# Kernel tuning notes

Measured on AMD Instinct MI355X. Metric: run time of the kernel, lower is better.

## Reference

```python
import jax, jax.numpy as jnp
import numpy as np

B, LQ, LKV, H, D, HS = 8, 32, 4096, 16, 64, 1024
ROPE_THETA = 10000.0
MAX_POS = 2080


def setup_inputs() -> dict:
    key = jax.random.key(0)
    ks = jax.random.split(key, 7)
    scale = 0.02
    return {
        "hidden_states": jax.random.normal(ks[0], (B, LQ, HS), dtype=jnp.float32),
        "encoder_hidden_states": jax.random.normal(ks[1], (B, LKV, HS), dtype=jnp.float32),
        "position_ids_q": jax.random.randint(ks[2], (B, LQ), 0, MAX_POS, dtype=jnp.int64),
        "Wq": jax.random.normal(ks[3], (HS, HS), dtype=jnp.float32) * scale,
        "Wk": jax.random.normal(ks[4], (HS, HS), dtype=jnp.float32) * scale,
        "Wv": jax.random.normal(ks[5], (HS, HS), dtype=jnp.float32) * scale,
        "Wo": jax.random.normal(ks[6], (HS, HS), dtype=jnp.float32) * scale,
    }


def _rotate_half(x):
    x1, x2 = jnp.split(x, 2, axis=-1)
    return jnp.concatenate([-x2, x1], axis=-1)


def _rope_cos_sin(position_ids):
    # LLaMA-style rotary embedding: inv_freq over even dims, emb = [freqs, freqs]
    inv_freq = 1.0 / (ROPE_THETA ** (jnp.arange(0, D, 2, dtype=jnp.float32) / D))
    freqs = position_ids.astype(jnp.float32)[..., None] * inv_freq  # [B, LQ, D/2]
    emb = jnp.concatenate([freqs, freqs], axis=-1)                  # [B, LQ, D]
    # broadcast over heads: [B, 1, LQ, D]
    return jnp.cos(emb)[:, None], jnp.sin(emb)[:, None]


def reference(hidden_states, encoder_hidden_states, position_ids_q, Wq, Wk, Wv, Wo):
    bsz, q_len, _ = hidden_states.shape
    kv_len = encoder_hidden_states.shape[1]
    # projections (weights stored [in, out])
    q = hidden_states @ Wq                       # [B, LQ, HS]
    k = encoder_hidden_states @ Wk               # [B, LKV, HS]
    v = encoder_hidden_states @ Wv               # [B, LKV, HS]
    # split heads -> [B, H, L, D]
    q = q.reshape(bsz, q_len, H, D).transpose(0, 2, 1, 3)
    k = k.reshape(bsz, kv_len, H, D).transpose(0, 2, 1, 3)
    v = v.reshape(bsz, kv_len, H, D).transpose(0, 2, 1, 3)
    # RoPE applied to QUERY ONLY (per original module)
    cos, sin = _rope_cos_sin(position_ids_q)
    q = q * cos + _rotate_half(q) * sin
    # scaled dot-product cross attention
    scores = jnp.einsum("bhqd,bhkd->bhqk", q, k) / jnp.sqrt(jnp.asarray(D, q.dtype))
    attn = jax.nn.softmax(scores, axis=-1)
    out = jnp.einsum("bhqk,bhkd->bhqd", attn, v)  # [B, H, LQ, D]
    out = out.transpose(0, 2, 1, 3).reshape(bsz, q_len, HS)
    return out @ Wo
```

## Files before the change

kernel.cpp:

```cpp
#include <hip/hip_runtime.h>


typedef float  f32x4  __attribute__((ext_vector_type(4)));
typedef __bf16 bf16x8 __attribute__((ext_vector_type(8)));

__device__ __forceinline__ ushort f2b(float x) {
  union { float f; unsigned u; } v; v.f = x;
  unsigned r = (v.u + 0x7fffu + ((v.u >> 16) & 1u)) >> 16;
  return (ushort)r;
}
__device__ __forceinline__ float b2f(ushort h) {
  union { unsigned u; float f; } v; v.u = ((unsigned)h) << 16; return v.f;
}
__device__ __forceinline__ void unpack2(unsigned v, float& lo, float& hi) {
  union { unsigned u; float f; } a, b;
  a.u = v << 16; b.u = v & 0xffff0000u;
  lo = a.f; hi = b.f;
}
__device__ __forceinline__ unsigned packb(float a, float b) {
  return (unsigned)f2b(a) | ((unsigned)f2b(b) << 16);
}
__device__ __forceinline__ int swz(int r) { return (r & 3) ^ ((r >> 2) & 3); }

__device__ __forceinline__ void gload16(const void* g, void* l) {
  __builtin_amdgcn_global_load_lds(
      (const __attribute__((address_space(1))) void*)g,
      (__attribute__((address_space(3))) void*)l, 16, 0, 0);
}

__global__ __launch_bounds__(256) void pack_x(
    const float* __restrict__ X, ushort* __restrict__ Xp1, ushort* __restrict__ Xp2) {
  const int z = blockIdx.z, jb = blockIdx.y, cb = blockIdx.x;
  const int t = threadIdx.x;
  __shared__ ushort sT[128 * 72];

#pragma unroll
  for (int rep = 0; rep < 2; ++rep) {
    const int j  = rep * 64 + (t >> 2);
    const int c0 = (t & 3) << 4;
    const float4* src = (const float4*)(X + ((size_t)z * 4096 + jb * 128 + j) * 1024 + cb * 64 + c0);
#pragma unroll
    for (int q = 0; q < 4; ++q) {
      const float4 v = src[q];
      ushort4 w; w.x = f2b(v.x); w.y = f2b(v.y); w.z = f2b(v.z); w.w = f2b(v.w);
      *(ushort4*)&sT[j * 72 + c0 + q * 4] = w;
    }
  }
  __syncthreads();

  ushort* o1 = Xp1 + ((size_t)(z * 32 + jb) * 32 + cb * 2) * 4096;
#pragma unroll
  for (int q = 0; q < 4; ++q) {
    const int kih = q >> 1;
    const int r   = ((q & 1) << 6) + (t >> 2);
    const int p   = t & 3;
    const int lc  = p ^ swz(r);
    const uint4 v = *(const uint4*)&sT[r * 72 + kih * 32 + lc * 8];
    *(uint4*)&o1[(size_t)kih * 4096 + ((size_t)(q & 1) << 11) + (size_t)t * 8] = v;
  }

  ushort* o2 = Xp2 + (((size_t)(z * 8 + (cb >> 1)) * 128 + jb * 4) * 4096) + ((size_t)(cb & 1) << 11);
#pragma unroll
  for (int q = 0; q < 4; ++q) {
    const int cl = t >> 2;
    const int p2 = t & 3;
    const int lj = p2 ^ swz(cl);
    union { ushort u[8]; uint4 v; } pk;
#pragma unroll
    for (int jj = 0; jj < 8; ++jj) pk.u[jj] = sT[(q * 32 + lj * 8 + jj) * 72 + cl];
    *(uint4*)&o2[(size_t)q * 4096 + (size_t)t * 8] = pk.v;
  }
}

__global__ __launch_bounds__(256) void pack_w(
    const float* __restrict__ Wq, const float* __restrict__ Wk,
    const float* __restrict__ Wv, const float* __restrict__ Wo,
    ushort* __restrict__ WqT, ushort* __restrict__ Wkb,
    ushort* __restrict__ WvT, ushort* __restrict__ WoT) {
  const int wsel = blockIdx.z;
  const float* src = (wsel == 0) ? Wq : (wsel == 1) ? Wk : (wsel == 2) ? Wv : Wo;
  const int row0 = blockIdx.y << 6, col0 = blockIdx.x << 6;
  const int t = threadIdx.x;
  __shared__ ushort sT[64 * 72];
  const int r = t >> 2, c0 = (t & 3) << 4;

  union { ushort u[16]; uint4 v[2]; } pk;
  const float4* s4 = (const float4*)(src + (size_t)(row0 + r) * 1024 + col0 + c0);
#pragma unroll
  for (int q = 0; q < 4; ++q) {
    const float4 v = s4[q];
    pk.u[q*4+0] = f2b(v.x); pk.u[q*4+1] = f2b(v.y);
    pk.u[q*4+2] = f2b(v.z); pk.u[q*4+3] = f2b(v.w);
  }
  if (wsel == 1) {
    ushort* dst = Wkb + (size_t)(row0 + r) * 1024 + col0 + c0;
    *(uint4*)dst = pk.v[0];
    *(uint4*)(dst + 8) = pk.v[1];
  } else {
#pragma unroll
    for (int q = 0; q < 16; ++q) sT[r * 72 + c0 + q] = pk.u[q];
    __syncthreads();
    ushort* dst = (wsel == 0) ? WqT : (wsel == 2) ? WvT : WoT;
    union { ushort u[16]; uint4 v[2]; } o;
#pragma unroll
    for (int q = 0; q < 16; ++q) o.u[q] = sT[(c0 + q) * 72 + r];
    ushort* d = dst + (size_t)(col0 + r) * 1024 + row0 + c0;
    *(uint4*)d = o.v[0];
    *(uint4*)(d + 8) = o.v[1];
  }
}

__global__ __launch_bounds__(256) void qrope_gemm(
    const float* __restrict__ hs, const ushort* __restrict__ WqT,
    float* __restrict__ qP) {
  __shared__ alignas(16) ushort sA[128 * 40];
  __shared__ alignas(16) ushort sB[128 * 40];
  const int nt = blockIdx.x, mt = blockIdx.y, ks = blockIdx.z;
  const int m0 = mt << 7, n0 = nt << 7, kb = ks << 8;
  const int t = threadIdx.x;
  const int wave = t >> 6, lane = t & 63;
  const int wm = wave >> 1, wn = wave & 1;
  const int fr = lane & 15, fq = lane >> 4;
  const int r = t >> 1, sg = (t & 1) << 4;

  f32x4 acc[4][4];
#pragma unroll
  for (int a = 0; a < 4; ++a)
#pragma unroll
    for (int c = 0; c < 4; ++c) acc[a][c] = (f32x4){0.f, 0.f, 0.f, 0.f};

  for (int it = 0; it < 8; ++it) {
    const int k0 = kb + (it << 5);
    {
      const float4* s4 = (const float4*)(hs + (size_t)(m0 + r) * 1024 + k0 + sg);
      union { ushort u[16]; uint4 v[2]; } pk;
#pragma unroll
      for (int q = 0; q < 4; ++q) {
        const float4 v = s4[q];
        pk.u[q*4+0] = f2b(v.x); pk.u[q*4+1] = f2b(v.y);
        pk.u[q*4+2] = f2b(v.z); pk.u[q*4+3] = f2b(v.w);
      }
      *(uint4*)&sA[r * 40 + sg]     = pk.v[0];
      *(uint4*)&sA[r * 40 + sg + 8] = pk.v[1];
    }
    {
      const uint4* s4 = (const uint4*)(WqT + (size_t)(n0 + r) * 1024 + k0 + sg);
      *(uint4*)&sB[r * 40 + sg]     = s4[0];
      *(uint4*)&sB[r * 40 + sg + 8] = s4[1];
    }
    __syncthreads();
    bf16x8 aF[4], bF[4];
#pragma unroll
    for (int u = 0; u < 4; ++u) {
      aF[u] = *(const bf16x8*)&sA[((wm << 6) + (u << 4) + fr) * 40 + (fq << 3)];
      bF[u] = *(const bf16x8*)&sB[((wn << 6) + (u << 4) + fr) * 40 + (fq << 3)];
    }
#pragma unroll
    for (int mi = 0; mi < 4; ++mi)
#pragma unroll
      for (int ni = 0; ni < 4; ++ni)
        acc[mi][ni] = __builtin_amdgcn_mfma_f32_16x16x32_bf16(
            aF[mi], bF[ni], acc[mi][ni], 0, 0, 0);
    __syncthreads();
  }
  float* dst = qP + (size_t)ks * 262144;
#pragma unroll
  for (int mi = 0; mi < 4; ++mi)
#pragma unroll
    for (int ni = 0; ni < 4; ++ni)
#pragma unroll
      for (int rr = 0; rr < 4; ++rr) {
        const int row = m0 + (wm << 6) + (mi << 4) + (fq << 2) + rr;
        const int col = n0 + (wn << 6) + (ni << 4) + fr;
        dst[(size_t)row * 1024 + col] = acc[mi][ni][rr];
      }
}

__global__ __launch_bounds__(256) void qk_rope_gemm(
    const float* __restrict__ qP, const ushort* __restrict__ Wkb,
    const int* __restrict__ pos, ushort* __restrict__ qk) {
  __shared__ float s_qf[32 * 68];
  __shared__ alignas(16) ushort sA[32 * 72];
  __shared__ alignas(16) ushort sB[256 * 72];
  const int nc = blockIdx.x, h = blockIdx.y, b = blockIdx.z;
  const int t = threadIdx.x;
  const int i = t >> 3, d0 = (t & 7) << 3;

  {
    float s[8];
#pragma unroll
    for (int j = 0; j < 8; ++j) s[j] = 0.f;
#pragma unroll
    for (int p = 0; p < 4; ++p) {
      const float* base = qP + (size_t)p * 262144 + (size_t)(b * 32 + i) * 1024 + h * 64 + d0;
      const float4 a0 = *(const float4*)base;
      const float4 a1 = *(const float4*)(base + 4);
      s[0]+=a0.x; s[1]+=a0.y; s[2]+=a0.z; s[3]+=a0.w;
      s[4]+=a1.x; s[5]+=a1.y; s[6]+=a1.z; s[7]+=a1.w;
    }
#pragma unroll
    for (int j = 0; j < 8; ++j) s_qf[i * 68 + d0 + j] = s[j];
  }
#pragma unroll
  for (int p = 0; p < 8; ++p) {
    const int rr = (t >> 3) + p * 32, seg = (t & 7) << 3;
    *(uint4*)&sB[rr * 72 + seg] =
        *(const uint4*)(Wkb + (size_t)(nc * 256 + rr) * 1024 + h * 64 + seg);
  }
  __syncthreads();

  {
    unsigned oddor = 0;
    for (int j = 1; j < 256; j += 2) oddor |= (unsigned)pos[j];
    const int m = b * 32 + i;
    const int p = (oddor == 0) ? pos[2 * m] : pos[m];
    const float pf = (float)p;
    union { ushort u16[8]; uint4 v; } o;
#pragma unroll
    for (int j = 0; j < 8; ++j) {
      const int d = d0 + j;
      const int f = d & 31;
      const float inv = powf(10000.0f, -(float)f * (1.0f / 32.0f));
      float sn, cs; sincosf(pf * inv, &sn, &cs);
      const float x  = s_qf[i * 68 + d];
      const float xp = s_qf[i * 68 + (d ^ 32)];
      const float v  = (d < 32) ? (x * cs - xp * sn) : (x * cs + xp * sn);
      o.u16[j] = f2b(v * 0.125f);
    }
    *(uint4*)&sA[i * 72 + d0] = o.v;
  }
  __syncthreads();

  const int wave = t >> 6, lane = t & 63;
  const int fr = lane & 15, fq = lane >> 4;
  f32x4 acc[2][4];
#pragma unroll
  for (int a = 0; a < 2; ++a)
#pragma unroll
    for (int c = 0; c < 4; ++c) acc[a][c] = (f32x4){0.f, 0.f, 0.f, 0.f};

#pragma unroll
  for (int ki = 0; ki < 2; ++ki) {
    bf16x8 aF[2], bF[4];
#pragma unroll
    for (int mi = 0; mi < 2; ++mi)
      aF[mi] = *(const bf16x8*)&sA[((mi << 4) + fr) * 72 + (ki << 5) + (fq << 3)];
#pragma unroll
    for (int ni = 0; ni < 4; ++ni)
      bF[ni] = *(const bf16x8*)&sB[((wave << 6) + (ni << 4) + fr) * 72 + (ki << 5) + (fq << 3)];
#pragma unroll
    for (int mi = 0; mi < 2; ++mi)
#pragma unroll
      for (int ni = 0; ni < 4; ++ni)
        acc[mi][ni] = __builtin_amdgcn_mfma_f32_16x16x32_bf16(
            aF[mi], bF[ni], acc[mi][ni], 0, 0, 0);
  }
#pragma unroll
  for (int mi = 0; mi < 2; ++mi)
#pragma unroll
    for (int ni = 0; ni < 4; ++ni)
#pragma unroll
      for (int rr = 0; rr < 4; ++rr) {
        const int row = h * 32 + (mi << 4) + (fq << 2) + rr;
        const int col = nc * 256 + (wave << 6) + (ni << 4) + fr;
        qk[((size_t)b * 512 + row) * 1024 + col] = f2b(acc[mi][ni][rr]);
      }
}

__global__ __launch_bounds__(256) void gemm1(
    const ushort* __restrict__ qk, const ushort* __restrict__ Xp1,
    ushort* __restrict__ Sc, float2* __restrict__ pstat) {
  __shared__ alignas(16) ushort sA[8192];
  __shared__ alignas(16) ushort sB[8192];
  __shared__ float sMx[256], sSm[256];
  const int z = blockIdx.x, nty = blockIdx.y, mt = blockIdx.z;
  const int tid = threadIdx.x;
  const int wave = tid >> 6, lane = tid & 63;
  const int wm = wave >> 1, wn = wave & 1;
  const int fr = lane & 15, fq = lane >> 4;
  const int sfr = swz(fr);

  const ushort* Ab = qk + ((size_t)z * 512 + mt * 128) * 1024;
  const ushort* Bb = Xp1 + ((size_t)(z * 32 + nty) * 32) * 4096;

  int arow[4], aoff[4];
#pragma unroll
  for (int j = 0; j < 4; ++j) {
    const int rowA = ((wave & 1) << 6) + (j << 4) + (lane >> 2);
    arow[j] = rowA;
    aoff[j] = ((wave >> 1) << 5) + (((lane & 3) ^ swz(rowA)) << 3);
  }

  f32x4 acc[4][4];
#pragma unroll
  for (int a = 0; a < 4; ++a)
#pragma unroll
    for (int c = 0; c < 4; ++c) acc[a][c] = (f32x4){0.f, 0.f, 0.f, 0.f};

  for (int it = 0; it < 16; ++it) {
    const int k0 = it << 6;
#pragma unroll
    for (int j = 0; j < 4; ++j) {
      gload16(Bb + (size_t)it * 8192 + wave * 2048 + j * 512 + lane * 8,
              &sB[wave * 2048 + j * 512]);
      gload16(Ab + (size_t)arow[j] * 1024 + k0 + aoff[j],
              &sA[wave * 2048 + j * 512]);
    }
    __syncthreads();
#pragma unroll
    for (int kk = 0; kk < 2; ++kk) {
      bf16x8 aF[4], bF[4];
#pragma unroll
      for (int u = 0; u < 4; ++u) {
        aF[u] = *(const bf16x8*)&sA[kk * 4096 + ((wm << 6) + (u << 4) + fr) * 32 + ((fq ^ sfr) << 3)];
        bF[u] = *(const bf16x8*)&sB[kk * 4096 + ((wn << 6) + (u << 4) + fr) * 32 + ((fq ^ sfr) << 3)];
      }
#pragma unroll
      for (int mi = 0; mi < 4; ++mi)
#pragma unroll
        for (int ni = 0; ni < 4; ++ni)
          acc[mi][ni] = __builtin_amdgcn_mfma_f32_16x16x32_bf16(
              aF[mi], bF[ni], acc[mi][ni], 0, 0, 0);
    }
    __syncthreads();
  }

  ushort* ScB = Sc + (size_t)(z * 4 + mt) * 524288;
#pragma unroll
  for (int mi = 0; mi < 4; ++mi)
#pragma unroll
    for (int ni = 0; ni < 4; ++ni)
#pragma unroll
      for (int r = 0; r < 4; ++r) {
        const int row = (wm << 6) + (mi << 4) + (fq << 2) + r;
        const int col = (wn << 6) + (ni << 4) + fr;
        const int ki  = (nty << 2) + (col >> 5);
        const int p   = ((col >> 3) & 3) ^ r ^ fq;
        const ushort hb = f2b(acc[mi][ni][r]);
        ScB[(size_t)ki * 4096 + row * 32 + p * 8 + (fr & 7)] = hb;
        acc[mi][ni][r] = b2f(hb);
      }

#pragma unroll
  for (int mi = 0; mi < 4; ++mi)
#pragma unroll
    for (int r = 0; r < 4; ++r) {
      float m4 = fmaxf(fmaxf(acc[mi][0][r], acc[mi][1][r]),
                       fmaxf(acc[mi][2][r], acc[mi][3][r]));
#pragma unroll
      for (int o = 1; o < 16; o <<= 1) m4 = fmaxf(m4, __shfl_xor(m4, o));
      float s4 = __expf(acc[mi][0][r] - m4) + __expf(acc[mi][1][r] - m4) +
                 __expf(acc[mi][2][r] - m4) + __expf(acc[mi][3][r] - m4);
#pragma unroll
      for (int o = 1; o < 16; o <<= 1) s4 += __shfl_xor(s4, o);
      if (fr == 0) {
        const int row = (wm << 6) + (mi << 4) + (fq << 2) + r;
        sMx[row * 2 + wn] = m4;
        sSm[row * 2 + wn] = s4;
      }
    }
  __syncthreads();
  if (tid < 128) {
    const float m0 = sMx[tid * 2], m1 = sMx[tid * 2 + 1];
    const float M = fmaxf(m0, m1);
    const float S = sSm[tid * 2] * __expf(m0 - M) + sSm[tid * 2 + 1] * __expf(m1 - M);
    pstat[((size_t)(z * 512 + mt * 128 + tid)) * 32 + nty] = make_float2(M, S);
  }
}

__global__ __launch_bounds__(256) void combine_stats(
    const float2* __restrict__ pstat, float2* __restrict__ stats2) {
  const int g = blockIdx.x * 256 + threadIdx.x;
  const float2* p = pstat + (size_t)g * 32;
  float M = -1e30f;
#pragma unroll
  for (int i = 0; i < 32; ++i) M = fmaxf(M, p[i].x);
  float S = 0.f;
#pragma unroll
  for (int i = 0; i < 32; ++i) S += p[i].y * __expf(p[i].x - M);
  stats2[g] = make_float2(M, 1.0f / S);
}

__global__ __launch_bounds__(256) void gemm2f(
    const ushort* __restrict__ Sc, const ushort* __restrict__ Xp2,
    const float2* __restrict__ stats2, float* __restrict__ P) {
  __shared__ alignas(16) ushort sA[8192];
  __shared__ alignas(16) ushort sB[8192];
  const int z = blockIdx.x, nty = blockIdx.y;
  const int mt = blockIdx.z & 3, s = blockIdx.z >> 2;
  const int tid = threadIdx.x;
  const int wave = tid >> 6, lane = tid & 63;
  const int wm = wave >> 1, wn = wave & 1;
  const int fr = lane & 15, fq = lane >> 4;
  const int sfr = swz(fr);

  const ushort* Ab = Sc + (size_t)(z * 4 + mt) * 524288 + (size_t)s * 262144;
  const ushort* Bb = Xp2 + ((size_t)(z * 8 + nty) * 128 + s * 64) * 4096;

  const float2 st0 = stats2[z * 512 + mt * 128 + (tid >> 2)];
  const float2 st1 = stats2[z * 512 + mt * 128 + 64 + (tid >> 2)];

  f32x4 acc[4][4];
#pragma unroll
  for (int a = 0; a < 4; ++a)
#pragma unroll
    for (int c = 0; c < 4; ++c) acc[a][c] = (f32x4){0.f, 0.f, 0.f, 0.f};

  for (int it = 0; it < 32; ++it) {
#pragma unroll
    for (int j = 0; j < 4; ++j)
      gload16(Bb + (size_t)it * 8192 + wave * 2048 + j * 512 + lane * 8,
              &sB[wave * 2048 + j * 512]);
#pragma unroll
    for (int j = 0; j < 4; ++j) {
      const uint4 v = *(const uint4*)(Ab + (size_t)it * 8192 + j * 2048 + tid * 8);
      const float M   = (j & 1) ? st1.x : st0.x;
      const float inv = (j & 1) ? st1.y : st0.y;
      float x0,x1,x2,x3,x4,x5,x6,x7;
      unpack2(v.x, x0, x1); unpack2(v.y, x2, x3);
      unpack2(v.z, x4, x5); unpack2(v.w, x6, x7);
      uint4 o;
      o.x = packb(__expf(x0 - M) * inv, __expf(x1 - M) * inv);
      o.y = packb(__expf(x2 - M) * inv, __expf(x3 - M) * inv);
      o.z = packb(__expf(x4 - M) * inv, __expf(x5 - M) * inv);
      o.w = packb(__expf(x6 - M) * inv, __expf(x7 - M) * inv);
      *(uint4*)&sA[j * 2048 + tid * 8] = o;
    }
    __syncthreads();
#pragma unroll
    for (int kk = 0; kk < 2; ++kk) {
      bf16x8 aF[4], bF[4];
#pragma unroll
      for (int u = 0; u < 4; ++u) {
        aF[u] = *(const bf16x8*)&sA[kk * 4096 + ((wm << 6) + (u << 4) + fr) * 32 + ((fq ^ sfr) << 3)];
        bF[u] = *(const bf16x8*)&sB[kk * 4096 + ((wn << 6) + (u << 4) + fr) * 32 + ((fq ^ sfr) << 3)];
      }
#pragma unroll
      for (int mi = 0; mi < 4; ++mi)
#pragma unroll
        for (int ni = 0; ni < 4; ++ni)
          acc[mi][ni] = __builtin_amdgcn_mfma_f32_16x16x32_bf16(
              aF[mi], bF[ni], acc[mi][ni], 0, 0, 0);
    }
    __syncthreads();
  }

  float* Pb = P + (((size_t)(s * 8 + z) * 512) + mt * 128) * 1024 + nty * 128;
#pragma unroll
  for (int mi = 0; mi < 4; ++mi)
#pragma unroll
    for (int ni = 0; ni < 4; ++ni)
#pragma unroll
      for (int r = 0; r < 4; ++r) {
        const int row = (wm << 6) + (mi << 4) + (fq << 2) + r;
        const int col = (wn << 6) + (ni << 4) + fr;
        Pb[(size_t)row * 1024 + col] = acc[mi][ni][r];
      }
}

__global__ __launch_bounds__(256) void ctxwv_gemm(
    const float* __restrict__ P, const ushort* __restrict__ WvT,
    float* __restrict__ P2) {
  __shared__ alignas(16) ushort sA[32 * 264];
  __shared__ alignas(16) ushort sB[64 * 264];
  const int ks = blockIdx.x, h = blockIdx.y, b = blockIdx.z;
  const int kb = ks << 8;
  const int t = threadIdx.x;
#pragma unroll
  for (int q = 0; q < 4; ++q) {
    const int i = t >> 3, seg = ((t & 7) + q * 8) << 3;
    const float* p0 = P + ((size_t)(0 * 8 + b) * 512 + h * 32 + i) * 1024 + kb + seg;
    const float* p1 = P + ((size_t)(1 * 8 + b) * 512 + h * 32 + i) * 1024 + kb + seg;
    const float4 a0 = *(const float4*)p0,       a1 = *(const float4*)(p0 + 4);
    const float4 b0 = *(const float4*)p1,       b1 = *(const float4*)(p1 + 4);
    uint4 o;
    o.x = packb(a0.x + b0.x, a0.y + b0.y);
    o.y = packb(a0.z + b0.z, a0.w + b0.w);
    o.z = packb(a1.x + b1.x, a1.y + b1.y);
    o.w = packb(a1.z + b1.z, a1.w + b1.w);
    *(uint4*)&sA[i * 264 + seg] = o;
  }
#pragma unroll
  for (int p = 0; p < 8; ++p) {
    const int rr = (t >> 3) + (p & 1) * 32;
    const int seg = ((t & 7) + (p >> 1) * 8) << 3;
    *(uint4*)&sB[rr * 264 + seg] =
        *(const uint4*)(WvT + (size_t)(h * 64 + rr) * 1024 + kb + seg);
  }
  __syncthreads();

  const int wave = t >> 6, lane = t & 63;
  const int fr = lane & 15, fq = lane >> 4;
  f32x4 acc[2];
  acc[0] = (f32x4){0.f, 0.f, 0.f, 0.f};
  acc[1] = (f32x4){0.f, 0.f, 0.f, 0.f};

#pragma unroll
  for (int ki = 0; ki < 8; ++ki) {
    bf16x8 bFr = *(const bf16x8*)&sB[((wave << 4) + fr) * 264 + (ki << 5) + (fq << 3)];
#pragma unroll
    for (int mi = 0; mi < 2; ++mi) {
      bf16x8 aF = *(const bf16x8*)&sA[((mi << 4) + fr) * 264 + (ki << 5) + (fq << 3)];
      acc[mi] = __builtin_amdgcn_mfma_f32_16x16x32_bf16(aF, bFr, acc[mi], 0, 0, 0);
    }
  }
  float* dst = P2 + (size_t)ks * 262144;
#pragma unroll
  for (int mi = 0; mi < 2; ++mi)
#pragma unroll
    for (int rr = 0; rr < 4; ++rr) {
      const int row = b * 32 + (mi << 4) + (fq << 2) + rr;
      const int col = h * 64 + (wave << 4) + fr;
      dst[(size_t)row * 1024 + col] = acc[mi][rr];
    }
}

__global__ __launch_bounds__(256) void out_gemm(
    const float* __restrict__ P2, const ushort* __restrict__ WoT,
    float* __restrict__ O4) {
  __shared__ alignas(16) ushort sA[128 * 40];
  __shared__ alignas(16) ushort sB[128 * 40];
  const int nt = blockIdx.x, mt = blockIdx.y, ks = blockIdx.z;
  const int m0 = mt << 7, n0 = nt << 7, kb = ks << 8;
  const int t = threadIdx.x;
  const int wave = t >> 6, lane = t & 63;
  const int wm = wave >> 1, wn = wave & 1;
  const int fr = lane & 15, fq = lane >> 4;
  const int r = t >> 1, sg = (t & 1) << 4;

  f32x4 acc[4][4];
#pragma unroll
  for (int a = 0; a < 4; ++a)
#pragma unroll
    for (int c = 0; c < 4; ++c) acc[a][c] = (f32x4){0.f, 0.f, 0.f, 0.f};

  for (int it = 0; it < 8; ++it) {
    const int k0 = kb + (it << 5);
    {
      float s[16];
#pragma unroll
      for (int j = 0; j < 16; ++j) s[j] = 0.f;
#pragma unroll
      for (int p = 0; p < 4; ++p) {
        const float* base = P2 + (size_t)p * 262144 + (size_t)(m0 + r) * 1024 + k0 + sg;
#pragma unroll
        for (int q = 0; q < 4; ++q) {
          const float4 v = *(const float4*)(base + q * 4);
          s[q*4+0] += v.x; s[q*4+1] += v.y; s[q*4+2] += v.z; s[q*4+3] += v.w;
        }
      }
      uint4 o0, o1;
      o0.x = packb(s[0], s[1]);   o0.y = packb(s[2], s[3]);
      o0.z = packb(s[4], s[5]);   o0.w = packb(s[6], s[7]);
      o1.x = packb(s[8], s[9]);   o1.y = packb(s[10], s[11]);
      o1.z = packb(s[12], s[13]); o1.w = packb(s[14], s[15]);
      *(uint4*)&sA[r * 40 + sg]     = o0;
      *(uint4*)&sA[r * 40 + sg + 8] = o1;
    }
    {
      const uint4* s4 = (const uint4*)(WoT + (size_t)(n0 + r) * 1024 + k0 + sg);
      *(uint4*)&sB[r * 40 + sg]     = s4[0];
      *(uint4*)&sB[r * 40 + sg + 8] = s4[1];
    }
    __syncthreads();
    bf16x8 aF[4], bF[4];
#pragma unroll
    for (int u = 0; u < 4; ++u) {
      aF[u] = *(const bf16x8*)&sA[((wm << 6) + (u << 4) + fr) * 40 + (fq << 3)];
      bF[u] = *(const bf16x8*)&sB[((wn << 6) + (u << 4) + fr) * 40 + (fq << 3)];
    }
#pragma unroll
    for (int mi = 0; mi < 4; ++mi)
#pragma unroll
      for (int ni = 0; ni < 4; ++ni)
        acc[mi][ni] = __builtin_amdgcn_mfma_f32_16x16x32_bf16(
            aF[mi], bF[ni], acc[mi][ni], 0, 0, 0);
    __syncthreads();
  }
  float* dst = O4 + (size_t)ks * 262144;
#pragma unroll
  for (int mi = 0; mi < 4; ++mi)
#pragma unroll
    for (int ni = 0; ni < 4; ++ni)
#pragma unroll
      for (int rr = 0; rr < 4; ++rr) {
        const int row = m0 + (wm << 6) + (mi << 4) + (fq << 2) + rr;
        const int col = n0 + (wn << 6) + (ni << 4) + fr;
        dst[(size_t)row * 1024 + col] = acc[mi][ni][rr];
      }
}

__global__ __launch_bounds__(256) void sum_out4(
    const float* __restrict__ O4, float* __restrict__ out) {
  const size_t i4 = ((size_t)blockIdx.x * 256 + threadIdx.x) * 4;
  float4 acc = *(const float4*)(O4 + i4);
#pragma unroll
  for (int p = 1; p < 4; ++p) {
    const float4 v = *(const float4*)(O4 + (size_t)p * 262144 + i4);
    acc.x += v.x; acc.y += v.y; acc.z += v.z; acc.w += v.w;
  }
  *(float4*)(out + i4) = acc;
}

extern "C" void kernel_launch(void* const* d_in, const int* in_sizes, int n_in,
                              void* d_out, int out_size, void* d_ws, size_t ws_size,
                              hipStream_t stream) {
  const float* hs  = (const float*)d_in[0];
  const float* enc = (const float*)d_in[1];
  const int*   pos = (const int*)d_in[2];
  const float* Wq  = (const float*)d_in[3];
  const float* Wk  = (const float*)d_in[4];
  const float* Wv  = (const float*)d_in[5];
  const float* Wo  = (const float*)d_in[6];
  float* out = (float*)d_out;

  char* w = (char*)d_ws;
  ushort* Xp1  = (ushort*)w;
  float*  P    = (float*)w;
  w += (size_t)67108864;
  ushort* Xp2  = (ushort*)w;
  float*  P2   = (float*)w;
  w += (size_t)67108864;
  ushort* qk   = (ushort*)w; w += (size_t)8388608;
  ushort* Sc   = (ushort*)w; w += (size_t)33554432;
  float2* pstat  = (float2*)w; w += (size_t)1048576;
  float2* stats2 = (float2*)w; w += (size_t)32768;
  float*  qP   = (float*)w;
  float*  O4   = (float*)w;
  w += (size_t)4194304;
  ushort* WqT = (ushort*)w; w += (size_t)2097152;
  ushort* Wkb = (ushort*)w; w += (size_t)2097152;
  ushort* WvT = (ushort*)w; w += (size_t)2097152;
  ushort* WoT = (ushort*)w; w += (size_t)2097152;

  pack_x<<<dim3(16, 32, 8), 256, 0, stream>>>(enc, Xp1, Xp2);
  pack_w<<<dim3(16, 16, 4), 256, 0, stream>>>(Wq, Wk, Wv, Wo, WqT, Wkb, WvT, WoT);
  qrope_gemm<<<dim3(8, 2, 4), 256, 0, stream>>>(hs, WqT, qP);
  qk_rope_gemm<<<dim3(4, 16, 8), 256, 0, stream>>>(qP, Wkb, pos, qk);
  gemm1<<<dim3(8, 32, 4), 256, 0, stream>>>(qk, Xp1, Sc, pstat);
  combine_stats<<<16, 256, 0, stream>>>(pstat, stats2);
  gemm2f<<<dim3(8, 8, 8), 256, 0, stream>>>(Sc, Xp2, stats2, P);
  ctxwv_gemm<<<dim3(4, 16, 8), 256, 0, stream>>>(P, WvT, P2);
  out_gemm<<<dim3(8, 2, 4), 256, 0, stream>>>(P2, WoT, O4);
  sum_out4<<<256, 256, 0, stream>>>(O4, out);
}
```

Before: 442.1 us.

## Apply softmax in a separate pass so the PV GEMM loads probabilities straight into LDS

Result: faster. 423.5 us (-4.2%).

```diff
diff --git a/kernel.cpp b/kernel.cpp
--- a/kernel.cpp
+++ b/kernel.cpp
@@ -28,85 +28,83 @@
       (__attribute__((address_space(3))) void*)l, 16, 0, 0);
 }
 
-__global__ __launch_bounds__(256) void pack_x(
-    const float* __restrict__ X, ushort* __restrict__ Xp1, ushort* __restrict__ Xp2) {
-  const int z = blockIdx.z, jb = blockIdx.y, cb = blockIdx.x;
-  const int t = threadIdx.x;
-  __shared__ ushort sT[128 * 72];
-
-#pragma unroll
-  for (int rep = 0; rep < 2; ++rep) {
-    const int j  = rep * 64 + (t >> 2);
-    const int c0 = (t & 3) << 4;
-    const float4* src = (const float4*)(X + ((size_t)z * 4096 + jb * 128 + j) * 1024 + cb * 64 + c0);
-#pragma unroll
-    for (int q = 0; q < 4; ++q) {
-      const float4 v = src[q];
-      ushort4 w; w.x = f2b(v.x); w.y = f2b(v.y); w.z = f2b(v.z); w.w = f2b(v.w);
-      *(ushort4*)&sT[j * 72 + c0 + q * 4] = w;
-    }
-  }
-  __syncthreads();
-
-  ushort* o1 = Xp1 + ((size_t)(z * 32 + jb) * 32 + cb * 2) * 4096;
-#pragma unroll
-  for (int q = 0; q < 4; ++q) {
-    const int kih = q >> 1;
-    const int r   = ((q & 1) << 6) + (t >> 2);
-    const int p   = t & 3;
-    const int lc  = p ^ swz(r);
-    const uint4 v = *(const uint4*)&sT[r * 72 + kih * 32 + lc * 8];
-    *(uint4*)&o1[(size_t)kih * 4096 + ((size_t)(q & 1) << 11) + (size_t)t * 8] = v;
-  }
-
-  ushort* o2 = Xp2 + (((size_t)(z * 8 + (cb >> 1)) * 128 + jb * 4) * 4096) + ((size_t)(cb & 1) << 11);
-#pragma unroll
-  for (int q = 0; q < 4; ++q) {
-    const int cl = t >> 2;
-    const int p2 = t & 3;
-    const int lj = p2 ^ swz(cl);
-    union { ushort u[8]; uint4 v; } pk;
-#pragma unroll
-    for (int jj = 0; jj < 8; ++jj) pk.u[jj] = sT[(q * 32 + lj * 8 + jj) * 72 + cl];
-    *(uint4*)&o2[(size_t)q * 4096 + (size_t)t * 8] = pk.v;
-  }
-}
-
-__global__ __launch_bounds__(256) void pack_w(
+__global__ __launch_bounds__(256) void pack_all(
+    const float* __restrict__ X, ushort* __restrict__ Xp1, ushort* __restrict__ Xp2,
     const float* __restrict__ Wq, const float* __restrict__ Wk,
     const float* __restrict__ Wv, const float* __restrict__ Wo,
     ushort* __restrict__ WqT, ushort* __restrict__ Wkb,
     ushort* __restrict__ WvT, ushort* __restrict__ WoT) {
-  const int wsel = blockIdx.z;
-  const float* src = (wsel == 0) ? Wq : (wsel == 1) ? Wk : (wsel == 2) ? Wv : Wo;
-  const int row0 = blockIdx.y << 6, col0 = blockIdx.x << 6;
   const int t = threadIdx.x;
-  __shared__ ushort sT[64 * 72];
-  const int r = t >> 2, c0 = (t & 3) << 4;
-
-  union { ushort u[16]; uint4 v[2]; } pk;
-  const float4* s4 = (const float4*)(src + (size_t)(row0 + r) * 1024 + col0 + c0);
-#pragma unroll
-  for (int q = 0; q < 4; ++q) {
-    const float4 v = s4[q];
-    pk.u[q*4+0] = f2b(v.x); pk.u[q*4+1] = f2b(v.y);
-    pk.u[q*4+2] = f2b(v.z); pk.u[q*4+3] = f2b(v.w);
-  }
-  if (wsel == 1) {
-    ushort* dst = Wkb + (size_t)(row0 + r) * 1024 + col0 + c0;
-    *(uint4*)dst = pk.v[0];
-    *(uint4*)(dst + 8) = pk.v[1];
+  if (blockIdx.z < 8) {
+    const int z = blockIdx.z, jb = blockIdx.y, cb = blockIdx.x;
+    __shared__ ushort sT[128 * 72];
+#pragma unroll
+    for (int rep = 0; rep < 2; ++rep) {
+      const int j  = rep * 64 + (t >> 2);
+      const int c0 = (t & 3) << 4;
+      const float4* src = (const float4*)(X + ((size_t)z * 4096 + jb * 128 + j) * 1024 + cb * 64 + c0);
+#pragma unroll
+      for (int q = 0; q < 4; ++q) {
+        const float4 v = src[q];
+        ushort4 w; w.x = f2b(v.x); w.y = f2b(v.y); w.z = f2b(v.z); w.w = f2b(v.w);
+        *(ushort4*)&sT[j * 72 + c0 + q * 4] = w;
+      }
+    }
+    __syncthreads();
+
+    ushort* o1 = Xp1 + ((size_t)(z * 32 + jb) * 32 + cb * 2) * 4096;
+#pragma unroll
+    for (int q = 0; q < 4; ++q) {
+      const int kih = q >> 1;
+      const int r   = ((q & 1) << 6) + (t >> 2);
+      const int p   = t & 3;
+      const int lc  = p ^ swz(r);
+      const uint4 v = *(const uint4*)&sT[r * 72 + kih * 32 + lc * 8];
+      *(uint4*)&o1[(size_t)kih * 4096 + ((size_t)(q & 1) << 11) + (size_t)t * 8] = v;
+    }
+
+    ushort* o2 = Xp2 + (((size_t)(z * 8 + (cb >> 1)) * 128 + jb * 4) * 4096) + ((size_t)(cb & 1) << 11);
+#pragma unroll
+    for (int q = 0; q < 4; ++q) {
+      const int cl = t >> 2;
+      const int p2 = t & 3;
+      const int lj = p2 ^ swz(cl);
+      union { ushort u[8]; uint4 v; } pk;
+#pragma unroll
+      for (int jj = 0; jj < 8; ++jj) pk.u[jj] = sT[(q * 32 + lj * 8 + jj) * 72 + cl];
+      *(uint4*)&o2[(size_t)q * 4096 + (size_t)t * 8] = pk.v;
+    }
   } else {
-#pragma unroll
-    for (int q = 0; q < 16; ++q) sT[r * 72 + c0 + q] = pk.u[q];
-    __syncthreads();
-    ushort* dst = (wsel == 0) ? WqT : (wsel == 2) ? WvT : WoT;
-    union { ushort u[16]; uint4 v[2]; } o;
-#pragma unroll
-    for (int q = 0; q < 16; ++q) o.u[q] = sT[(c0 + q) * 72 + r];
-    ushort* d = dst + (size_t)(col0 + r) * 1024 + row0 + c0;
-    *(uint4*)d = o.v[0];
-    *(uint4*)(d + 8) = o.v[1];
+    const int wsel = (blockIdx.z - 8) * 2 + (blockIdx.y >> 4);
+    const float* src = (wsel == 0) ? Wq : (wsel == 1) ? Wk : (wsel == 2) ? Wv : Wo;
+    const int row0 = (blockIdx.y & 15) << 6, col0 = blockIdx.x << 6;
+    __shared__ ushort sW[64 * 72];
+    const int r = t >> 2, c0 = (t & 3) << 4;
+
+    union { ushort u[16]; uint4 v[2]; } pk;
+    const float4* s4 = (const float4*)(src + (size_t)(row0 + r) * 1024 + col0 + c0);
+#pragma unroll
+    for (int q = 0; q < 4; ++q) {
+      const float4 v = s4[q];
+      pk.u[q*4+0] = f2b(v.x); pk.u[q*4+1] = f2b(v.y);
+      pk.u[q*4+2] = f2b(v.z); pk.u[q*4+3] = f2b(v.w);
+    }
+    if (wsel == 1) {
+      ushort* dst = Wkb + (size_t)(row0 + r) * 1024 + col0 + c0;
+      *(uint4*)dst = pk.v[0];
+      *(uint4*)(dst + 8) = pk.v[1];
+    } else {
+#pragma unroll
+      for (int q = 0; q < 16; ++q) sW[r * 72 + c0 + q] = pk.u[q];
+      __syncthreads();
+      ushort* dst = (wsel == 0) ? WqT : (wsel == 2) ? WvT : WoT;
+      union { ushort u[16]; uint4 v[2]; } o;
+#pragma unroll
+      for (int q = 0; q < 16; ++q) o.u[q] = sW[(c0 + q) * 72 + r];
+      ushort* d = dst + (size_t)(col0 + r) * 1024 + row0 + c0;
+      *(uint4*)d = o.v[0];
+      *(uint4*)(d + 8) = o.v[1];
+    }
   }
 }
 
@@ -211,7 +209,8 @@
 
   {
     unsigned oddor = 0;
-    for (int j = 1; j < 256; j += 2) oddor |= (unsigned)pos[j];
+#pragma unroll
+    for (int j = 1; j < 32; j += 2) oddor |= (unsigned)pos[j];
     const int m = b * 32 + i;
     const int p = (oddor == 0) ? pos[2 * m] : pos[m];
     const float pf = (float)p;
@@ -368,22 +367,51 @@
   }
 }
 
-__global__ __launch_bounds__(256) void combine_stats(
-    const float2* __restrict__ pstat, float2* __restrict__ stats2) {
-  const int g = blockIdx.x * 256 + threadIdx.x;
-  const float2* p = pstat + (size_t)g * 32;
-  float M = -1e30f;
-#pragma unroll
-  for (int i = 0; i < 32; ++i) M = fmaxf(M, p[i].x);
-  float S = 0.f;
-#pragma unroll
-  for (int i = 0; i < 32; ++i) S += p[i].y * __expf(p[i].x - M);
-  stats2[g] = make_float2(M, 1.0f / S);
-}
-
-__global__ __launch_bounds__(256) void gemm2f(
-    const ushort* __restrict__ Sc, const ushort* __restrict__ Xp2,
-    const float2* __restrict__ stats2, float* __restrict__ P) {
+__global__ __launch_bounds__(256) void softmax_apply2(
+    ushort* __restrict__ Sc, const float2* __restrict__ pstat) {
+  __shared__ float sM[128], sI[128];
+  const int zmt = blockIdx.x, kg = blockIdx.y;
+  const int t = threadIdx.x;
+  if (t < 128) {
+    const float2* p = pstat + ((size_t)zmt * 128 + t) * 32;
+    float M = -1e30f;
+#pragma unroll
+    for (int i = 0; i < 32; ++i) M = fmaxf(M, p[i].x);
+    float S = 0.f;
+#pragma unroll
+    for (int i = 0; i < 32; ++i) S += p[i].y * __expf(p[i].x - M);
+    sM[t] = M; sI[t] = 1.0f / S;
+  }
+  __syncthreads();
+  const int r = t >> 1;
+  const float M = sM[r], inv = sI[r];
+  ushort* base = Sc + ((size_t)zmt * 128 + kg * 8) * 4096 + t * 16;
+#pragma unroll
+  for (int kt = 0; kt < 8; ++kt) {
+    uint4 v0 = *(uint4*)base;
+    uint4 v1 = *(uint4*)(base + 8);
+    float x0,x1,x2,x3,x4,x5,x6,x7;
+    unpack2(v0.x, x0, x1); unpack2(v0.y, x2, x3);
+    unpack2(v0.z, x4, x5); unpack2(v0.w, x6, x7);
+    v0.x = packb(__expf(x0 - M) * inv, __expf(x1 - M) * inv);
+    v0.y = packb(__expf(x2 - M) * inv, __expf(x3 - M) * inv);
+    v0.z = packb(__expf(x4 - M) * inv, __expf(x5 - M) * inv);
+    v0.w = packb(__expf(x6 - M) * inv, __expf(x7 - M) * inv);
+    unpack2(v1.x, x0, x1); unpack2(v1.y, x2, x3);
+    unpack2(v1.z, x4, x5); unpack2(v1.w, x6, x7);
+    v1.x = packb(__expf(x0 - M) * inv, __expf(x1 - M) * inv);
+    v1.y = packb(__expf(x2 - M) * inv, __expf(x3 - M) * inv);
+    v1.z = packb(__expf(x4 - M) * inv, __expf(x5 - M) * inv);
+    v1.w = packb(__expf(x6 - M) * inv, __expf(x7 - M) * inv);
+    *(uint4*)base = v0;
+    *(uint4*)(base + 8) = v1;
+    base += 4096;
+  }
+}
+
+__global__ __launch_bounds__(256) void gemm2p(
+    const ushort* __restrict__ At, const ushort* __restrict__ Xp2,
+    float* __restrict__ P) {
   __shared__ alignas(16) ushort sA[8192];
   __shared__ alignas(16) ushort sB[8192];
   const int z = blockIdx.x, nty = blockIdx.y;
@@ -394,12 +422,9 @@
   const int fr = lane & 15, fq = lane >> 4;
   const int sfr = swz(fr);
 
-  const ushort* Ab = Sc + (size_t)(z * 4 + mt) * 524288 + (size_t)s * 262144;
+  const ushort* Ab = At + (size_t)(z * 4 + mt) * 524288 + (size_t)s * 262144;
   const ushort* Bb = Xp2 + ((size_t)(z * 8 + nty) * 128 + s * 64) * 4096;
 
-  const float2 st0 = stats2[z * 512 + mt * 128 + (tid >> 2)];
-  const float2 st1 = stats2[z * 512 + mt * 128 + 64 + (tid >> 2)];
-
   f32x4 acc[4][4];
 #pragma unroll
   for (int a = 0; a < 4; ++a)
@@ -408,23 +433,11 @@
 
   for (int it = 0; it < 32; ++it) {
 #pragma unroll
-    for (int j = 0; j < 4; ++j)
+    for (int j = 0; j < 4; ++j) {
       gload16(Bb + (size_t)it * 8192 + wave * 2048 + j * 512 + lane * 8,
               &sB[wave * 2048 + j * 512]);
-#pragma unroll
-    for (int j = 0; j < 4; ++j) {
-      const uint4 v = *(const uint4*)(Ab + (size_t)it * 8192 + j * 2048 + tid * 8);
-      const float M   = (j & 1) ? st1.x : st0.x;
-      const float inv = (j & 1) ? st1.y : st0.y;
-      float x0,x1,x2,x3,x4,x5,x6,x7;
-      unpack2(v.x, x0, x1); unpack2(v.y, x2, x3);
-      unpack2(v.z, x4, x5); unpack2(v.w, x6, x7);
-      uint4 o;
-      o.x = packb(__expf(x0 - M) * inv, __expf(x1 - M) * inv);
-      o.y = packb(__expf(x2 - M) * inv, __expf(x3 - M) * inv);
-      o.z = packb(__expf(x4 - M) * inv, __expf(x5 - M) * inv);
-      o.w = packb(__expf(x6 - M) * inv, __expf(x7 - M) * inv);
-      *(uint4*)&sA[j * 2048 + tid * 8] = o;
+      gload16(Ab + (size_t)it * 8192 + wave * 2048 + j * 512 + lane * 8,
+              &sA[wave * 2048 + j * 512]);
     }
     __syncthreads();
 #pragma unroll
@@ -624,7 +637,6 @@
   ushort* qk   = (ushort*)w; w += (size_t)8388608;
   ushort* Sc   = (ushort*)w; w += (size_t)33554432;
   float2* pstat  = (float2*)w; w += (size_t)1048576;
-  float2* stats2 = (float2*)w; w += (size_t)32768;
   float*  qP   = (float*)w;
   float*  O4   = (float*)w;
   w += (size_t)4194304;
@@ -633,13 +645,13 @@
   ushort* WvT = (ushort*)w; w += (size_t)2097152;
   ushort* WoT = (ushort*)w; w += (size_t)2097152;
 
-  pack_x<<<dim3(16, 32, 8), 256, 0, stream>>>(enc, Xp1, Xp2);
-  pack_w<<<dim3(16, 16, 4), 256, 0, stream>>>(Wq, Wk, Wv, Wo, WqT, Wkb, WvT, WoT);
+  pack_all<<<dim3(16, 32, 10), 256, 0, stream>>>(enc, Xp1, Xp2,
+      Wq, Wk, Wv, Wo, WqT, Wkb, WvT, WoT);
   qrope_gemm<<<dim3(8, 2, 4), 256, 0, stream>>>(hs, WqT, qP);
   qk_rope_gemm<<<dim3(4, 16, 8), 256, 0, stream>>>(qP, Wkb, pos, qk);
   gemm1<<<dim3(8, 32, 4), 256, 0, stream>>>(qk, Xp1, Sc, pstat);
-  combine_stats<<<16, 256, 0, stream>>>(pstat, stats2);
-  gemm2f<<<dim3(8, 8, 8), 256, 0, stream>>>(Sc, Xp2, stats2, P);
+  softmax_apply2<<<dim3(32, 16), 256, 0, stream>>>(Sc, pstat);
+  gemm2p<<<dim3(8, 8, 8), 256, 0, stream>>>(Sc, Xp2, P);
   ctxwv_gemm<<<dim3(4, 16, 8), 256, 0, stream>>>(P, WvT, P2);
   out_gemm<<<dim3(8, 2, 4), 256, 0, stream>>>(P2, WoT, O4);
   sum_out4<<<256, 256, 0, stream>>>(O4, out);
```
